# Optimization experiments

Hardware: AMD Instinct MI355X
Metric: run time of the kernel (lower is better)

Reference implementation:

```python
import jax, jax.numpy as jnp
import numpy as np

N_NODES = 50000

def _add_self_loops(edge_index, n):
    loop = jnp.arange(n, dtype=edge_index.dtype)
    src = jnp.concatenate([edge_index[0], loop])
    dst = jnp.concatenate([edge_index[1], loop])
    return src, dst

def _gcn_conv(x, src, dst, W, b, n):
    h = x @ W
    deg = jax.ops.segment_sum(jnp.ones_like(dst, dtype=h.dtype), dst, num_segments=n)
    inv_sqrt = jnp.where(deg > 0, jax.lax.rsqrt(deg), 0.0)
    coef = inv_sqrt[src] * inv_sqrt[dst]            # [E]
    msg = h[src] * coef[:, None]                     # [E, hidden]
    return jax.ops.segment_sum(msg, dst, num_segments=n) + b

def _gat_conv(x, src, dst, W, att_src, att_dst, b, n, heads, out_dim):
    # PyG GATConv, concat=False -> mean over heads; self-loops already added
    h = (x @ W).reshape(n, heads, out_dim)           # [N, H, F]
    a_src = jnp.sum(h * att_src, axis=-1)            # [N, H]
    a_dst = jnp.sum(h * att_dst, axis=-1)            # [N, H]
    e = a_src[src] + a_dst[dst]                      # [E, H]
    e = jax.nn.leaky_relu(e, negative_slope=0.2)
    # neighborhood softmax over edges grouped by destination
    m = jax.ops.segment_max(e, dst, num_segments=n)  # [N, H]
    ex = jnp.exp(e - m[dst])
    denom = jax.ops.segment_sum(ex, dst, num_segments=n)
    alpha = ex / denom[dst]                          # [E, H]
    out = jax.ops.segment_sum(h[src] * alpha[:, :, None], dst, num_segments=n)  # [N, H, F]
    return out.mean(axis=1) + b                      # concat=False -> head mean

def setup_inputs() -> dict:
    key = jax.random.key(0)
    ks = jax.random.split(key, 12)
    n, input_dim, hidden, output_dim, heads = N_NODES, 128, 128, 64, 2
    gat_out = hidden // 2
    x = jax.random.normal(ks[0], (n, input_dim), dtype=jnp.float32)
    edge_index = jax.random.randint(ks[1], (2, 800000), 0, n, dtype=jnp.int64)
    s = lambda fi, fo: float(np.sqrt(1.0 / fi))
    W1 = jax.random.normal(ks[2], (input_dim, hidden), dtype=jnp.float32) * s(input_dim, hidden)
    b1 = jnp.zeros((hidden,), dtype=jnp.float32)
    Wg = jax.random.normal(ks[3], (hidden, heads * gat_out), dtype=jnp.float32) * s(hidden, gat_out)
    att_src = jax.random.normal(ks[4], (heads, gat_out), dtype=jnp.float32) * s(gat_out, 1)
    att_dst = jax.random.normal(ks[5], (heads, gat_out), dtype=jnp.float32) * s(gat_out, 1)
    bg = jnp.zeros((gat_out,), dtype=jnp.float32)
    W3 = jax.random.normal(ks[6], (gat_out, output_dim), dtype=jnp.float32) * s(gat_out, output_dim)
    b3 = jnp.zeros((output_dim,), dtype=jnp.float32)
    return {"x": x, "edge_index": edge_index, "W1": W1, "b1": b1, "Wg": Wg,
            "att_src": att_src, "att_dst": att_dst, "bg": bg, "W3": W3, "b3": b3}

def reference(x, edge_index, W1, b1, Wg, att_src, att_dst, bg, W3, b3):
    n = x.shape[0]
    heads, gat_out = att_src.shape
    src, dst = _add_self_loops(edge_index, n)
    # dropout is identity in eval mode
    h = _gcn_conv(x, src, dst, W1, b1, n)
    h = jax.nn.relu(h)
    h = _gat_conv(h, src, dst, Wg, att_src, att_dst, bg, n, heads, gat_out)
    h = jax.nn.elu(h)
    return _gcn_conv(h, src, dst, W3, b3, n)
```

## Files before the change

### kernel.cpp

```cpp
#include <hip/hip_runtime.h>
#include <hip/hip_bf16.h>
#include <math.h>

#define N_NODES 50000
#define E0      800000
#define E_TOT   (E0 + N_NODES)
#define SCAP    512

using bf16 = __hip_bfloat16;
typedef __attribute__((ext_vector_type(8))) short bfrag;
typedef __attribute__((ext_vector_type(4))) float ffrag;

static __device__ __forceinline__ float bfu2f_lo(unsigned u){ return __uint_as_float(u << 16); }
static __device__ __forceinline__ float bfu2f_hi(unsigned u){ return __uint_as_float(u & 0xffff0000u); }
static __device__ __forceinline__ float us2f(unsigned short u){ return __uint_as_float((unsigned)u << 16); }

static __device__ __forceinline__ unsigned packbf(float a, float b){
    bf16 x = __float2bfloat16(a), y = __float2bfloat16(b);
    unsigned short ux = *reinterpret_cast<unsigned short*>(&x);
    unsigned short uy = *reinterpret_cast<unsigned short*>(&y);
    return ((unsigned)uy << 16) | ux;
}

static __device__ __forceinline__ int detect_f32(const unsigned* xu){
    int lane = threadIdx.x & 63;
    unsigned ex = (xu[lane] >> 7) & 0xFF;
    return (__ballot(ex < 100 || ex > 140) != 0ULL);
}
static __device__ __forceinline__ int detect_i32(const int* ei){
    int lane = threadIdx.x & 63;
    return (__ballot(ei[2 * lane + 1] != 0) != 0ULL);
}

static __device__ __forceinline__ float ldany(const void* p, int i, int isf32){
    return isf32 ? ((const float*)p)[i] : __bfloat162float(((const bf16*)p)[i]);
}

__global__ void k_convert(const void* __restrict__ xv,
                          const void* W1, const void* Wg, const void* W3,
                          const void* b1, const void* bg, const void* b3,
                          const void* as_, const void* ad_,
                          bf16* __restrict__ W1p, bf16* __restrict__ Wgp,
                          bf16* __restrict__ W3p, float* __restrict__ vecf,
                          bf16* __restrict__ xb, int* __restrict__ deg){
    const int NXB = (N_NODES * 128 + 255) / 256;
    int b = blockIdx.x, t = threadIdx.x;
    if (b >= 148 + NXB){
        int i = (b - 148 - NXB) * 256 + t;
        if (i < N_NODES) deg[i] = 0;
        return;
    }
    int isf = detect_f32((const unsigned*)xv);
    if (b >= 148){
        int i = (b - 148) * 256 + t;
        if (i < N_NODES * 128) xb[i] = __float2bfloat16(ldany(xv, i, isf));
        return;
    }
    if (b < 16){
        int dd = b * 256 + t;
        int j  = dd & 7;
        int L  = (dd >> 3) & 63;
        int kc = (dd >> 9) & 1;
        int ct = dd >> 10;
        int k = kc * 32 + ((L >> 4) << 3) + j;
        int n = ct * 16 + (L & 15);
        W3p[dd] = __float2bfloat16(ldany(W3, k * 64 + n, isf));
    }
    else if (b < 18){
        int i = (b - 16) * 256 + t;
        float v;
        if      (i < 128) v = ldany(b1,  i,       isf);
        else if (i < 192) v = ldany(bg,  i - 128, isf);
        else if (i < 256) v = ldany(b3,  i - 192, isf);
        else if (i < 384) v = ldany(as_, i - 256, isf);
        else              v = ldany(ad_, i - 384, isf);
        vecf[i] = v;
    } else {
        int d = (b - 18) * 256 + t;
        const void* Wsrc = (d < 16384) ? W1 : Wg;
        bf16* Wdst = (d < 16384) ? W1p : Wgp;
        int dd = d & 16383;
        int j  = dd & 7;
        int L  = (dd >> 3) & 63;
        int kc = (dd >> 9) & 3;
        int ct = dd >> 11;
        int k = kc * 32 + ((L >> 4) << 3) + j;
        int n = ct * 16 + (L & 15);
        Wdst[dd] = __float2bfloat16(ldany(Wsrc, k * 128 + n, isf));
    }
}


static __device__ __forceinline__ int load_dst(const int* ei, int e, int is32){
    if (e >= E0) return e - E0;
    return is32 ? ei[E0 + e] : (int)((const long long*)ei)[E0 + e];
}
static __device__ __forceinline__ int load_src(const int* ei, int e, int is32){
    if (e >= E0) return e - E0;
    return is32 ? ei[e] : (int)((const long long*)ei)[e];
}

__global__ void k_count(const int* __restrict__ ei, int* __restrict__ deg,
                        int* __restrict__ rank){
    int is32 = detect_i32(ei);
    int e = blockIdx.x * blockDim.x + threadIdx.x;
    if (e >= E_TOT) return;
    int dst = load_dst(ei, e, is32);
    int src = load_src(ei, e, is32);
    if ((unsigned)dst >= N_NODES || (unsigned)src >= N_NODES) return;
    rank[e] = atomicAdd(&deg[dst], 1);
}

__global__ void k_scanA(const int* __restrict__ deg, int* __restrict__ tmp, int* __restrict__ blk){
    __shared__ int s[256];
    int t = threadIdx.x;
    int i = blockIdx.x * 256 + t;
    int v = (i < N_NODES) ? deg[i] : 0;
    s[t] = v; __syncthreads();
    for (int off = 1; off < 256; off <<= 1){
        int x = (t >= off) ? s[t - off] : 0;
        __syncthreads();
        s[t] += x;
        __syncthreads();
    }
    if (t == 255) blk[blockIdx.x] = s[255];
    if (i < N_NODES) tmp[i] = s[t] - v;
}

__global__ void k_scanC(int* __restrict__ row_ptr, const int* __restrict__ blk,
                        const int* __restrict__ deg, float* __restrict__ inv_sqrt,
                        int nb){
    __shared__ int s[256];
    int t = threadIdx.x;
    int B = blockIdx.x;
    s[t] = (t < nb && t < B) ? blk[t] : 0;
    __syncthreads();
    for (int off = 128; off; off >>= 1){
        if (t < off) s[t] += s[t + off];
        __syncthreads();
    }
    int base = s[0];
    int i = B * 256 + t;
    if (i < N_NODES){
        row_ptr[i] += base;
        int d = deg[i];
        inv_sqrt[i] = (d > 0) ? rsqrtf((float)d) : 0.0f;
    }
    if (i == 0) row_ptr[N_NODES] = E_TOT;
}

__global__ void k_fill(const int* __restrict__ ei, const int* __restrict__ row_ptr,
                       const float* __restrict__ isq, const int* __restrict__ rank,
                       int2* __restrict__ ecr){
    int is32 = detect_i32(ei);
    int e = blockIdx.x * blockDim.x + threadIdx.x;
    if (e >= E_TOT) return;
    int dst = load_dst(ei, e, is32);
    int src = load_src(ei, e, is32);
    if ((unsigned)dst >= N_NODES || (unsigned)src >= N_NODES) return;
    int pos = row_ptr[dst] + rank[e];
    float c = isq[dst] * isq[src];
    ecr[pos] = make_int2(src, __float_as_int(c));
}

__global__ __launch_bounds__(256, 2) void k_gather(
        const ushort4* __restrict__ xb4, const int* __restrict__ rp,
        const int2* __restrict__ ecr, uint2* __restrict__ Xa){
    __shared__ int   scsr[SCAP];
    __shared__ float scf[SCAP];
    int n0 = blockIdx.x * 4;
    int b0 = rp[n0];
    int tot  = rp[n0 + 4] - b0;
    int stot = min(tot, SCAP);
    for (int i = threadIdx.x; i < stot; i += 256){
        int2 ev = ecr[b0 + i];
        scsr[i] = ev.x;
        scf[i]  = __int_as_float(ev.y);
    }
    __syncthreads();

    int w    = threadIdx.x >> 6;
    int half = (threadIdx.x >> 5) & 1;
    int fz   = threadIdx.x & 31;
    int n = n0 + w;
    float a0 = 0.f, a1 = 0.f, a2 = 0.f, a3 = 0.f;
    int b = rp[n] - b0, e = rp[n + 1] - b0;
    int elim = min(e, stot);
    #pragma unroll 4
    for (int i = b + half; i < elim; i += 2){
        int s = scsr[i];
        float c = scf[i];
        ushort4 v = xb4[(size_t)s * 32 + fz];
        a0 += c * us2f(v.x);  a1 += c * us2f(v.y);
        a2 += c * us2f(v.z);  a3 += c * us2f(v.w);
    }
    int start = max(b, stot);
    int i0 = start + (((b + half) ^ start) & 1);
    for (int i = i0; i < e; i += 2){
        int2 ev = ecr[b0 + i];
        float c = __int_as_float(ev.y);
        ushort4 v = xb4[(size_t)ev.x * 32 + fz];
        a0 += c * us2f(v.x);  a1 += c * us2f(v.y);
        a2 += c * us2f(v.z);  a3 += c * us2f(v.w);
    }
    a0 += __shfl_xor(a0, 32, 64);  a1 += __shfl_xor(a1, 32, 64);
    a2 += __shfl_xor(a2, 32, 64);  a3 += __shfl_xor(a3, 32, 64);
    if (half == 0)
        Xa[(size_t)n * 32 + fz] = make_uint2(packbf(a0, a1), packbf(a2, a3));
}

template<int EPI>
__global__ __launch_bounds__(512) void k_gemm_mfma(
        const bf16* __restrict__ A, const bf16* __restrict__ Wp,
        const float* __restrict__ vecf, bf16* __restrict__ O,
        float* __restrict__ aS, float* __restrict__ aD){
    __shared__ float sA[16][8];
    __shared__ float sD[16][8];
    int wid  = threadIdx.x >> 6;
    int lane = threadIdx.x & 63;
    int n0 = blockIdx.x * 16;
    int m = lane & 15, q = lane >> 4;

    const bfrag* Ap = (const bfrag*)(A + (size_t)(n0 + m) * 128);
    const bfrag* Bp = (const bfrag*)Wp + (size_t)wid * 256 + lane;

    ffrag c = {0.f, 0.f, 0.f, 0.f};
    #pragma unroll
    for (int kc = 0; kc < 4; ++kc){
        bfrag af = Ap[kc * 4 + q];
        bfrag bf = Bp[kc * 64];
        c = __builtin_amdgcn_mfma_f32_16x16x32_bf16(af, bf, c, 0, 0, 0);
    }
    __syncthreads();

    int col = wid * 16 + m;
    if (EPI == 0){
        float bb = vecf[col];
        #pragma unroll
        for (int r = 0; r < 4; ++r){
            int row = n0 + q * 4 + r;
            O[(size_t)row * 128 + col] = __float2bfloat16(fmaxf(c[r] + bb, 0.f));
        }
    } else {
        int f = col & 63, h = col >> 6;
        float as_v = vecf[256 + h * 64 + f];
        float ad_v = vecf[384 + h * 64 + f];
        float ps[4], pd[4];
        #pragma unroll
        for (int r = 0; r < 4; ++r){
            int row = n0 + q * 4 + r;
            O[(size_t)row * 128 + f * 2 + h] = __float2bfloat16(c[r]);
            ps[r] = c[r] * as_v;
            pd[r] = c[r] * ad_v;
        }
        #pragma unroll
        for (int off = 1; off < 16; off <<= 1){
            #pragma unroll
            for (int r = 0; r < 4; ++r){
                ps[r] += __shfl_xor(ps[r], off, 64);
                pd[r] += __shfl_xor(pd[r], off, 64);
            }
        }
        if (m == 0){
            #pragma unroll
            for (int r = 0; r < 4; ++r){
                int rl = q * 4 + r;
                sA[rl][wid] = ps[r];
                sD[rl][wid] = pd[r];
            }
        }
        __syncthreads();
        int t = threadIdx.x;
        if (t < 64){
            int rl = t >> 2, hh = (t >> 1) & 1, which = t & 1;
            const float (*S)[8] = which ? sD : sA;
            float v = S[rl][hh * 4 + 0] + S[rl][hh * 4 + 1]
                    + S[rl][hh * 4 + 2] + S[rl][hh * 4 + 3];
            float* dp = which ? aD : aS;
            dp[(size_t)(n0 + rl) * 2 + hh] = v;
        }
    }
}

__global__ __launch_bounds__(256) void k_gemm_z(
        const bf16* __restrict__ Y, const bf16* __restrict__ W3p,
        bf16* __restrict__ Z){
    int wid  = threadIdx.x >> 6;
    int lane = threadIdx.x & 63;
    int n0 = blockIdx.x * 16;
    int m = lane & 15, q = lane >> 4;

    const bfrag* Ap = (const bfrag*)(Y + (size_t)(n0 + m) * 64);
    const bfrag* Bp = (const bfrag*)W3p + (size_t)wid * 128 + lane;

    ffrag c = {0.f, 0.f, 0.f, 0.f};
    #pragma unroll
    for (int kc = 0; kc < 2; ++kc){
        bfrag af = Ap[kc * 4 + q];
        bfrag bf = Bp[kc * 64];
        c = __builtin_amdgcn_mfma_f32_16x16x32_bf16(af, bf, c, 0, 0, 0);
    }
    int col = wid * 16 + m;
    #pragma unroll
    for (int r = 0; r < 4; ++r){
        int row = n0 + q * 4 + r;
        Z[(size_t)row * 64 + col] = __float2bfloat16(c[r]);
    }
}

__global__ __launch_bounds__(256) void k_gat(
        const uint2* __restrict__ X2u2, const int* __restrict__ rp,
        const int2* __restrict__ ecr, const float2* __restrict__ a_src,
        const float2* __restrict__ a_dst, const float* __restrict__ vecf,
        unsigned* __restrict__ Yu){
    __shared__ int    scsr[SCAP];
    __shared__ float2 pe[SCAP];
    int n0 = blockIdx.x * 4;
    int b0 = rp[n0];
    int tot  = rp[n0 + 4] - b0;
    int stot = min(tot, SCAP);
    for (int i = threadIdx.x; i < stot; i += 256) scsr[i] = ecr[b0 + i].x;
    __syncthreads();

    int w    = threadIdx.x >> 6;
    int f    = threadIdx.x & 63;
    int half = (threadIdx.x >> 5) & 1;
    int fz   = threadIdx.x & 31;
    int n = n0 + w;
    float2 ad = a_dst[n];
    int b = rp[n] - b0, e = rp[n + 1] - b0;
    int elim = min(e, stot);

    for (int i = b + f; i < elim; i += 64){
        float2 av = a_src[scsr[i]];
        float e0 = av.x + ad.x, e1 = av.y + ad.y;
        e0 = (e0 > 0.f) ? e0 : 0.2f * e0;
        e1 = (e1 > 0.f) ? e1 : 0.2f * e1;
        pe[i] = make_float2(__expf(e0), __expf(e1));
    }

    float l0 = 0.f, l1 = 0.f;
    float o00 = 0.f, o01 = 0.f, o10 = 0.f, o11 = 0.f;
    #pragma unroll 4
    for (int i = b + half; i < elim; i += 2){
        float2 p = pe[i];
        uint2 v = X2u2[(size_t)scsr[i] * 32 + fz];
        l0  += p.x;                 l1  += p.y;
        o00 += p.x * bfu2f_lo(v.x); o01 += p.y * bfu2f_hi(v.x);
        o10 += p.x * bfu2f_lo(v.y); o11 += p.y * bfu2f_hi(v.y);
    }
    int start = max(b, stot);
    int i0 = start + (((b + half) ^ start) & 1);
    for (int i = i0; i < e; i += 2){
        int s = ecr[b0 + i].x;
        float2 av = a_src[s];
        uint2 v = X2u2[(size_t)s * 32 + fz];
        float e0 = av.x + ad.x, e1 = av.y + ad.y;
        e0 = (e0 > 0.f) ? e0 : 0.2f * e0;
        e1 = (e1 > 0.f) ? e1 : 0.2f * e1;
        float p0 = __expf(e0), p1 = __expf(e1);
        l0  += p0;                 l1  += p1;
        o00 += p0 * bfu2f_lo(v.x); o01 += p1 * bfu2f_hi(v.x);
        o10 += p0 * bfu2f_lo(v.y); o11 += p1 * bfu2f_hi(v.y);
    }
    l0  += __shfl_xor(l0, 32, 64);   l1  += __shfl_xor(l1, 32, 64);
    o00 += __shfl_xor(o00, 32, 64);  o01 += __shfl_xor(o01, 32, 64);
    o10 += __shfl_xor(o10, 32, 64);  o11 += __shfl_xor(o11, 32, 64);
    if (half == 0){
        float v0 = 0.5f * (o00 / l0 + o01 / l1) + vecf[128 + 2 * fz];
        float v1 = 0.5f * (o10 / l0 + o11 / l1) + vecf[128 + 2 * fz + 1];
        v0 = (v0 > 0.f) ? v0 : expm1f(v0);
        v1 = (v1 > 0.f) ? v1 : expm1f(v1);
        Yu[(size_t)n * 32 + fz] = packbf(v0, v1);
    }
}

__global__ __launch_bounds__(256) void k_gather_out(
        const unsigned* __restrict__ Zu, const int* __restrict__ rp,
        const int2* __restrict__ ecr, const float* __restrict__ vecf,
        float2* __restrict__ out2){
    __shared__ int   scsr[SCAP];
    __shared__ float scf[SCAP];
    int n0 = blockIdx.x * 4;
    int b0 = rp[n0];
    int tot  = rp[n0 + 4] - b0;
    int stot = min(tot, SCAP);
    for (int i = threadIdx.x; i < stot; i += 256){
        int2 ev = ecr[b0 + i];
        scsr[i] = ev.x;
        scf[i]  = __int_as_float(ev.y);
    }
    __syncthreads();

    int w    = threadIdx.x >> 6;
    int half = (threadIdx.x >> 5) & 1;
    int fz   = threadIdx.x & 31;
    int n = n0 + w;
    float a0 = 0.f, a1 = 0.f;
    int b = rp[n] - b0, e = rp[n + 1] - b0;
    int elim = min(e, stot);
    #pragma unroll 4
    for (int i = b + half; i < elim; i += 2){
        float c = scf[i];
        unsigned v = Zu[(size_t)scsr[i] * 32 + fz];
        a0 += c * bfu2f_lo(v);
        a1 += c * bfu2f_hi(v);
    }
    int start = max(b, stot);
    int i0 = start + (((b + half) ^ start) & 1);
    for (int i = i0; i < e; i += 2){
        int2 ev = ecr[b0 + i];
        float c = __int_as_float(ev.y);
        unsigned v = Zu[(size_t)ev.x * 32 + fz];
        a0 += c * bfu2f_lo(v);
        a1 += c * bfu2f_hi(v);
    }
    a0 += __shfl_xor(a0, 32, 64);
    a1 += __shfl_xor(a1, 32, 64);
    if (half == 0)
        out2[(size_t)n * 32 + fz] =
            make_float2(a0 + vecf[192 + 2 * fz], a1 + vecf[192 + 2 * fz + 1]);
}


extern "C" void kernel_launch(void* const* d_in, const int* in_sizes, int n_in,
                              void* d_out, int out_size, void* d_ws, size_t ws_size,
                              hipStream_t stream) {
    const void* x  = d_in[0];
    const int*  ei = (const int*)d_in[1];
    float* out = (float*)d_out;

    char* p = (char*)d_ws;
    auto alloc = [&](size_t bytes) -> void* {
        void* r = (void*)p;
        p += (bytes + 255) & ~(size_t)255;
        return r;
    };
    int*   deg      = (int*)  alloc((size_t)N_NODES * 4);
    int*   row_ptr  = (int*)  alloc((size_t)(N_NODES + 1) * 4);
    int*   blk      = (int*)  alloc(256 * 4);
    int*   rank     = (int*)  alloc((size_t)E_TOT * 4);
    int2*  ecr      = (int2*) alloc((size_t)E_TOT * 8);
    float* inv_sqrt = (float*)alloc((size_t)N_NODES * 4);
    float* a_src    = (float*)alloc((size_t)N_NODES * 2 * 4);
    float* a_dst    = (float*)alloc((size_t)N_NODES * 2 * 4);
    bf16*  W1p      = (bf16*) alloc(16384 * 2);
    bf16*  Wgp      = (bf16*) alloc(16384 * 2);
    bf16*  W3p      = (bf16*) alloc(4096 * 2);
    float* vecf     = (float*)alloc(512 * 4);
    bf16*  xb       = (bf16*) alloc((size_t)N_NODES * 128 * 2);
    bf16*  XA       = (bf16*) alloc((size_t)N_NODES * 128 * 2);
    bf16*  Y        = (bf16*) alloc((size_t)N_NODES * 64 * 2);
    bf16*  Z        = xb;

    const int NB_NODE = (N_NODES + 255) / 256;
    const int NB_EDGE = (E_TOT + 255) / 256;
    const int NXB     = (N_NODES * 128 + 255) / 256;
    const int NB_CONV = 148 + NXB + NB_NODE;

    k_convert<<<NB_CONV, 256, 0, stream>>>(x, d_in[2], d_in[4], d_in[8],
                                           d_in[3], d_in[7], d_in[9], d_in[5], d_in[6],
                                           W1p, Wgp, W3p, vecf, xb, deg);
    k_count<<<NB_EDGE, 256, 0, stream>>>(ei, deg, rank);
    k_scanA<<<NB_NODE, 256, 0, stream>>>(deg, row_ptr, blk);
    k_scanC<<<NB_NODE, 256, 0, stream>>>(row_ptr, blk, deg, inv_sqrt, NB_NODE);
    k_fill<<<NB_EDGE, 256, 0, stream>>>(ei, row_ptr, inv_sqrt, rank, ecr);

    k_gather<<<N_NODES / 4, 256, 0, stream>>>((const ushort4*)xb, row_ptr, ecr,
                                              (uint2*)XA);
    k_gemm_mfma<0><<<N_NODES / 16, 512, 0, stream>>>(XA, W1p, vecf, XA,
                                                     nullptr, nullptr);
    k_gemm_mfma<1><<<N_NODES / 16, 512, 0, stream>>>(XA, Wgp, vecf, XA,
                                                     a_src, a_dst);
    k_gat<<<N_NODES / 4, 256, 0, stream>>>((const uint2*)XA, row_ptr, ecr,
                                           (const float2*)a_src, (const float2*)a_dst,
                                           vecf, (unsigned*)Y);
    k_gemm_z<<<N_NODES / 16, 256, 0, stream>>>(Y, W3p, Z);
    k_gather_out<<<N_NODES / 4, 256, 0, stream>>>((const unsigned*)Z, row_ptr, ecr,
                                                  vecf, (float2*)out);
}
```

Baseline: 289.9 us.

## Widen gather loads to 16 bytes and split wave into four edge lanes

The three edge-gather kernels (GCN gather, GAT aggregation, output gather) now have each lane load wider vectors per source row (uint4 or uint2 instead of ushort4, uint2 or unsigned). The 64-lane wave is split into four groups of 16 lanes that process four edges at once, with a two-step shuffle reduction at the end. The input conversion is also vectorised to float4 loads and uint2 stores. The aim is fewer, wider memory transactions and more edge-level parallelism per wave. The cost is extra registers and shuffle work, and the gather kernel loses its explicit two-blocks-per-CU occupancy hint.

```diff
diff --git a/kernel.cpp b/kernel.cpp
--- a/kernel.cpp
+++ b/kernel.cpp
@@ -13,7 +13,6 @@
 
 static __device__ __forceinline__ float bfu2f_lo(unsigned u){ return __uint_as_float(u << 16); }
 static __device__ __forceinline__ float bfu2f_hi(unsigned u){ return __uint_as_float(u & 0xffff0000u); }
-static __device__ __forceinline__ float us2f(unsigned short u){ return __uint_as_float((unsigned)u << 16); }
 
 static __device__ __forceinline__ unsigned packbf(float a, float b){
     bf16 x = __float2bfloat16(a), y = __float2bfloat16(b);
@@ -43,7 +42,7 @@
                           bf16* __restrict__ W1p, bf16* __restrict__ Wgp,
                           bf16* __restrict__ W3p, float* __restrict__ vecf,
                           bf16* __restrict__ xb, int* __restrict__ deg){
-    const int NXB = (N_NODES * 128 + 255) / 256;
+    const int NXB = (N_NODES * 32 + 255) / 256;
     int b = blockIdx.x, t = threadIdx.x;
     if (b >= 148 + NXB){
         int i = (b - 148 - NXB) * 256 + t;
@@ -53,7 +52,14 @@
     int isf = detect_f32((const unsigned*)xv);
     if (b >= 148){
         int i = (b - 148) * 256 + t;
-        if (i < N_NODES * 128) xb[i] = __float2bfloat16(ldany(xv, i, isf));
+        if (i < N_NODES * 32){
+            if (isf){
+                float4 v = ((const float4*)xv)[i];
+                ((uint2*)xb)[i] = make_uint2(packbf(v.x, v.y), packbf(v.z, v.w));
+            } else {
+                ((uint2*)xb)[i] = ((const uint2*)xv)[i];
+            }
+        }
         return;
     }
     if (b < 16){
@@ -163,15 +169,14 @@
     ecr[pos] = make_int2(src, __float_as_int(c));
 }
 
-__global__ __launch_bounds__(256, 2) void k_gather(
-        const ushort4* __restrict__ xb4, const int* __restrict__ rp,
-        const int2* __restrict__ ecr, uint2* __restrict__ Xa){
+__global__ __launch_bounds__(256) void k_gather(
+        const uint4* __restrict__ xb16, const int* __restrict__ rp,
+        const int2* __restrict__ ecr, uint4* __restrict__ Xa16){
     __shared__ int   scsr[SCAP];
     __shared__ float scf[SCAP];
     int n0 = blockIdx.x * 4;
     int b0 = rp[n0];
-    int tot  = rp[n0 + 4] - b0;
-    int stot = min(tot, SCAP);
+    int stot = min(rp[n0 + 4] - b0, SCAP);
     for (int i = threadIdx.x; i < stot; i += 256){
         int2 ev = ecr[b0 + i];
         scsr[i] = ev.x;
@@ -179,34 +184,47 @@
     }
     __syncthreads();
 
-    int w    = threadIdx.x >> 6;
-    int half = (threadIdx.x >> 5) & 1;
-    int fz   = threadIdx.x & 31;
+    int w = threadIdx.x >> 6, lane = threadIdx.x & 63;
+    int q4 = lane >> 4, fz = lane & 15;
     int n = n0 + w;
-    float a0 = 0.f, a1 = 0.f, a2 = 0.f, a3 = 0.f;
+    float a0=0,a1=0,a2=0,a3=0,a4=0,a5=0,a6=0,a7=0;
     int b = rp[n] - b0, e = rp[n + 1] - b0;
     int elim = min(e, stot);
-    #pragma unroll 4
-    for (int i = b + half; i < elim; i += 2){
+    #pragma unroll 2
+    for (int i = b + q4; i < elim; i += 4){
         int s = scsr[i];
         float c = scf[i];
-        ushort4 v = xb4[(size_t)s * 32 + fz];
-        a0 += c * us2f(v.x);  a1 += c * us2f(v.y);
-        a2 += c * us2f(v.z);  a3 += c * us2f(v.w);
+        uint4 v = xb16[(size_t)s * 16 + fz];
+        a0 += c * bfu2f_lo(v.x);  a1 += c * bfu2f_hi(v.x);
+        a2 += c * bfu2f_lo(v.y);  a3 += c * bfu2f_hi(v.y);
+        a4 += c * bfu2f_lo(v.z);  a5 += c * bfu2f_hi(v.z);
+        a6 += c * bfu2f_lo(v.w);  a7 += c * bfu2f_hi(v.w);
     }
     int start = max(b, stot);
-    int i0 = start + (((b + half) ^ start) & 1);
-    for (int i = i0; i < e; i += 2){
+    int i0 = start + (((b + q4) - start) & 3);
+    for (int i = i0; i < e; i += 4){
         int2 ev = ecr[b0 + i];
         float c = __int_as_float(ev.y);
-        ushort4 v = xb4[(size_t)ev.x * 32 + fz];
-        a0 += c * us2f(v.x);  a1 += c * us2f(v.y);
-        a2 += c * us2f(v.z);  a3 += c * us2f(v.w);
-    }
-    a0 += __shfl_xor(a0, 32, 64);  a1 += __shfl_xor(a1, 32, 64);
-    a2 += __shfl_xor(a2, 32, 64);  a3 += __shfl_xor(a3, 32, 64);
-    if (half == 0)
-        Xa[(size_t)n * 32 + fz] = make_uint2(packbf(a0, a1), packbf(a2, a3));
+        uint4 v = xb16[(size_t)ev.x * 16 + fz];
+        a0 += c * bfu2f_lo(v.x);  a1 += c * bfu2f_hi(v.x);
+        a2 += c * bfu2f_lo(v.y);  a3 += c * bfu2f_hi(v.y);
+        a4 += c * bfu2f_lo(v.z);  a5 += c * bfu2f_hi(v.z);
+        a6 += c * bfu2f_lo(v.w);  a7 += c * bfu2f_hi(v.w);
+    }
+    a0 += __shfl_xor(a0, 32, 64);  a0 += __shfl_xor(a0, 16, 64);
+    a1 += __shfl_xor(a1, 32, 64);  a1 += __shfl_xor(a1, 16, 64);
+    a2 += __shfl_xor(a2, 32, 64);  a2 += __shfl_xor(a2, 16, 64);
+    a3 += __shfl_xor(a3, 32, 64);  a3 += __shfl_xor(a3, 16, 64);
+    a4 += __shfl_xor(a4, 32, 64);  a4 += __shfl_xor(a4, 16, 64);
+    a5 += __shfl_xor(a5, 32, 64);  a5 += __shfl_xor(a5, 16, 64);
+    a6 += __shfl_xor(a6, 32, 64);  a6 += __shfl_xor(a6, 16, 64);
+    a7 += __shfl_xor(a7, 32, 64);  a7 += __shfl_xor(a7, 16, 64);
+    if (lane < 16){
+        uint4 o;
+        o.x = packbf(a0, a1);  o.y = packbf(a2, a3);
+        o.z = packbf(a4, a5);  o.w = packbf(a6, a7);
+        Xa16[(size_t)n * 16 + fz] = o;
+    }
 }
 
 template<int EPI>
@@ -309,29 +327,26 @@
 }
 
 __global__ __launch_bounds__(256) void k_gat(
-        const uint2* __restrict__ X2u2, const int* __restrict__ rp,
+        const uint4* __restrict__ X2v, const int* __restrict__ rp,
         const int2* __restrict__ ecr, const float2* __restrict__ a_src,
         const float2* __restrict__ a_dst, const float* __restrict__ vecf,
-        unsigned* __restrict__ Yu){
+        uint2* __restrict__ Yu2){
     __shared__ int    scsr[SCAP];
     __shared__ float2 pe[SCAP];
     int n0 = blockIdx.x * 4;
     int b0 = rp[n0];
-    int tot  = rp[n0 + 4] - b0;
-    int stot = min(tot, SCAP);
+    int stot = min(rp[n0 + 4] - b0, SCAP);
     for (int i = threadIdx.x; i < stot; i += 256) scsr[i] = ecr[b0 + i].x;
     __syncthreads();
 
-    int w    = threadIdx.x >> 6;
-    int f    = threadIdx.x & 63;
-    int half = (threadIdx.x >> 5) & 1;
-    int fz   = threadIdx.x & 31;
+    int w = threadIdx.x >> 6, lane = threadIdx.x & 63;
+    int q4 = lane >> 4, fz = lane & 15;
     int n = n0 + w;
     float2 ad = a_dst[n];
     int b = rp[n] - b0, e = rp[n + 1] - b0;
     int elim = min(e, stot);
 
-    for (int i = b + f; i < elim; i += 64){
+    for (int i = b + lane; i < elim; i += 64){
         float2 av = a_src[scsr[i]];
         float e0 = av.x + ad.x, e1 = av.y + ad.y;
         e0 = (e0 > 0.f) ? e0 : 0.2f * e0;
@@ -340,21 +355,23 @@
     }
 
     float l0 = 0.f, l1 = 0.f;
-    float o00 = 0.f, o01 = 0.f, o10 = 0.f, o11 = 0.f;
-    #pragma unroll 4
-    for (int i = b + half; i < elim; i += 2){
+    float o00=0,o01=0, o10=0,o11=0, o20=0,o21=0, o30=0,o31=0;
+    #pragma unroll 2
+    for (int i = b + q4; i < elim; i += 4){
         float2 p = pe[i];
-        uint2 v = X2u2[(size_t)scsr[i] * 32 + fz];
-        l0  += p.x;                 l1  += p.y;
-        o00 += p.x * bfu2f_lo(v.x); o01 += p.y * bfu2f_hi(v.x);
-        o10 += p.x * bfu2f_lo(v.y); o11 += p.y * bfu2f_hi(v.y);
+        uint4 v = X2v[(size_t)scsr[i] * 16 + fz];
+        l0  += p.x;                  l1  += p.y;
+        o00 += p.x * bfu2f_lo(v.x);  o01 += p.y * bfu2f_hi(v.x);
+        o10 += p.x * bfu2f_lo(v.y);  o11 += p.y * bfu2f_hi(v.y);
+        o20 += p.x * bfu2f_lo(v.z);  o21 += p.y * bfu2f_hi(v.z);
+        o30 += p.x * bfu2f_lo(v.w);  o31 += p.y * bfu2f_hi(v.w);
     }
     int start = max(b, stot);
-    int i0 = start + (((b + half) ^ start) & 1);
-    for (int i = i0; i < e; i += 2){
+    int i0 = start + (((b + q4) - start) & 3);
+    for (int i = i0; i < e; i += 4){
         int s = ecr[b0 + i].x;
         float2 av = a_src[s];
-        uint2 v = X2u2[(size_t)s * 32 + fz];
+        uint4 v = X2v[(size_t)s * 16 + fz];
         float e0 = av.x + ad.x, e1 = av.y + ad.y;
         e0 = (e0 > 0.f) ? e0 : 0.2f * e0;
         e1 = (e1 > 0.f) ? e1 : 0.2f * e1;
@@ -362,29 +379,41 @@
         l0  += p0;                 l1  += p1;
         o00 += p0 * bfu2f_lo(v.x); o01 += p1 * bfu2f_hi(v.x);
         o10 += p0 * bfu2f_lo(v.y); o11 += p1 * bfu2f_hi(v.y);
-    }
-    l0  += __shfl_xor(l0, 32, 64);   l1  += __shfl_xor(l1, 32, 64);
-    o00 += __shfl_xor(o00, 32, 64);  o01 += __shfl_xor(o01, 32, 64);
-    o10 += __shfl_xor(o10, 32, 64);  o11 += __shfl_xor(o11, 32, 64);
-    if (half == 0){
-        float v0 = 0.5f * (o00 / l0 + o01 / l1) + vecf[128 + 2 * fz];
-        float v1 = 0.5f * (o10 / l0 + o11 / l1) + vecf[128 + 2 * fz + 1];
+        o20 += p0 * bfu2f_lo(v.z); o21 += p1 * bfu2f_hi(v.z);
+        o30 += p0 * bfu2f_lo(v.w); o31 += p1 * bfu2f_hi(v.w);
+    }
+    l0  += __shfl_xor(l0, 32, 64);   l0  += __shfl_xor(l0, 16, 64);
+    l1  += __shfl_xor(l1, 32, 64);   l1  += __shfl_xor(l1, 16, 64);
+    o00 += __shfl_xor(o00, 32, 64);  o00 += __shfl_xor(o00, 16, 64);
+    o01 += __shfl_xor(o01, 32, 64);  o01 += __shfl_xor(o01, 16, 64);
+    o10 += __shfl_xor(o10, 32, 64);  o10 += __shfl_xor(o10, 16, 64);
+    o11 += __shfl_xor(o11, 32, 64);  o11 += __shfl_xor(o11, 16, 64);
+    o20 += __shfl_xor(o20, 32, 64);  o20 += __shfl_xor(o20, 16, 64);
+    o21 += __shfl_xor(o21, 32, 64);  o21 += __shfl_xor(o21, 16, 64);
+    o30 += __shfl_xor(o30, 32, 64);  o30 += __shfl_xor(o30, 16, 64);
+    o31 += __shfl_xor(o31, 32, 64);  o31 += __shfl_xor(o31, 16, 64);
+    if (lane < 16){
+        float v0 = 0.5f * (o00 / l0 + o01 / l1) + vecf[128 + 4 * fz + 0];
+        float v1 = 0.5f * (o10 / l0 + o11 / l1) + vecf[128 + 4 * fz + 1];
+        float v2 = 0.5f * (o20 / l0 + o21 / l1) + vecf[128 + 4 * fz + 2];
+        float v3 = 0.5f * (o30 / l0 + o31 / l1) + vecf[128 + 4 * fz + 3];
         v0 = (v0 > 0.f) ? v0 : expm1f(v0);
         v1 = (v1 > 0.f) ? v1 : expm1f(v1);
-        Yu[(size_t)n * 32 + fz] = packbf(v0, v1);
+        v2 = (v2 > 0.f) ? v2 : expm1f(v2);
+        v3 = (v3 > 0.f) ? v3 : expm1f(v3);
+        Yu2[(size_t)n * 16 + fz] = make_uint2(packbf(v0, v1), packbf(v2, v3));
     }
 }
 
 __global__ __launch_bounds__(256) void k_gather_out(
-        const unsigned* __restrict__ Zu, const int* __restrict__ rp,
+        const uint2* __restrict__ Zu2, const int* __restrict__ rp,
         const int2* __restrict__ ecr, const float* __restrict__ vecf,
-        float2* __restrict__ out2){
+        float4* __restrict__ out4){
     __shared__ int   scsr[SCAP];
     __shared__ float scf[SCAP];
     int n0 = blockIdx.x * 4;
     int b0 = rp[n0];
-    int tot  = rp[n0 + 4] - b0;
-    int stot = min(tot, SCAP);
+    int stot = min(rp[n0 + 4] - b0, SCAP);
     for (int i = threadIdx.x; i < stot; i += 256){
         int2 ev = ecr[b0 + i];
         scsr[i] = ev.x;
@@ -392,34 +421,36 @@
     }
     __syncthreads();
 
-    int w    = threadIdx.x >> 6;
-    int half = (threadIdx.x >> 5) & 1;
-    int fz   = threadIdx.x & 31;
+    int w = threadIdx.x >> 6, lane = threadIdx.x & 63;
+    int q4 = lane >> 4, fz = lane & 15;
     int n = n0 + w;
-    float a0 = 0.f, a1 = 0.f;
+    float a0 = 0.f, a1 = 0.f, a2 = 0.f, a3 = 0.f;
     int b = rp[n] - b0, e = rp[n + 1] - b0;
     int elim = min(e, stot);
-    #pragma unroll 4
-    for (int i = b + half; i < elim; i += 2){
+    #pragma unroll 2
+    for (int i = b + q4; i < elim; i += 4){
         float c = scf[i];
-        unsigned v = Zu[(size_t)scsr[i] * 32 + fz];
-        a0 += c * bfu2f_lo(v);
-        a1 += c * bfu2f_hi(v);
+        uint2 v = Zu2[(size_t)scsr[i] * 16 + fz];
+        a0 += c * bfu2f_lo(v.x);  a1 += c * bfu2f_hi(v.x);
+        a2 += c * bfu2f_lo(v.y);  a3 += c * bfu2f_hi(v.y);
     }
     int start = max(b, stot);
-    int i0 = start + (((b + half) ^ start) & 1);
-    for (int i = i0; i < e; i += 2){
+    int i0 = start + (((b + q4) - start) & 3);
+    for (int i = i0; i < e; i += 4){
         int2 ev = ecr[b0 + i];
         float c = __int_as_float(ev.y);
-        unsigned v = Zu[(size_t)ev.x * 32 + fz];
-        a0 += c * bfu2f_lo(v);
-        a1 += c * bfu2f_hi(v);
-    }
-    a0 += __shfl_xor(a0, 32, 64);
-    a1 += __shfl_xor(a1, 32, 64);
-    if (half == 0)
-        out2[(size_t)n * 32 + fz] =
-            make_float2(a0 + vecf[192 + 2 * fz], a1 + vecf[192 + 2 * fz + 1]);
+        uint2 v = Zu2[(size_t)ev.x * 16 + fz];
+        a0 += c * bfu2f_lo(v.x);  a1 += c * bfu2f_hi(v.x);
+        a2 += c * bfu2f_lo(v.y);  a3 += c * bfu2f_hi(v.y);
+    }
+    a0 += __shfl_xor(a0, 32, 64);  a0 += __shfl_xor(a0, 16, 64);
+    a1 += __shfl_xor(a1, 32, 64);  a1 += __shfl_xor(a1, 16, 64);
+    a2 += __shfl_xor(a2, 32, 64);  a2 += __shfl_xor(a2, 16, 64);
+    a3 += __shfl_xor(a3, 32, 64);  a3 += __shfl_xor(a3, 16, 64);
+    if (lane < 16)
+        out4[(size_t)n * 16 + fz] = make_float4(
+            a0 + vecf[192 + 4 * fz + 0], a1 + vecf[192 + 4 * fz + 1],
+            a2 + vecf[192 + 4 * fz + 2], a3 + vecf[192 + 4 * fz + 3]);
 }
 
 
@@ -455,7 +486,7 @@
 
     const int NB_NODE = (N_NODES + 255) / 256;
     const int NB_EDGE = (E_TOT + 255) / 256;
-    const int NXB     = (N_NODES * 128 + 255) / 256;
+    const int NXB     = (N_NODES * 32 + 255) / 256;
     const int NB_CONV = 148 + NXB + NB_NODE;
 
     k_convert<<<NB_CONV, 256, 0, stream>>>(x, d_in[2], d_in[4], d_in[8],
@@ -466,16 +497,16 @@
     k_scanC<<<NB_NODE, 256, 0, stream>>>(row_ptr, blk, deg, inv_sqrt, NB_NODE);
     k_fill<<<NB_EDGE, 256, 0, stream>>>(ei, row_ptr, inv_sqrt, rank, ecr);
 
-    k_gather<<<N_NODES / 4, 256, 0, stream>>>((const ushort4*)xb, row_ptr, ecr,
-                                              (uint2*)XA);
+    k_gather<<<N_NODES / 4, 256, 0, stream>>>((const uint4*)xb, row_ptr, ecr,
+                                              (uint4*)XA);
     k_gemm_mfma<0><<<N_NODES / 16, 512, 0, stream>>>(XA, W1p, vecf, XA,
                                                      nullptr, nullptr);
     k_gemm_mfma<1><<<N_NODES / 16, 512, 0, stream>>>(XA, Wgp, vecf, XA,
                                                      a_src, a_dst);
-    k_gat<<<N_NODES / 4, 256, 0, stream>>>((const uint2*)XA, row_ptr, ecr,
+    k_gat<<<N_NODES / 4, 256, 0, stream>>>((const uint4*)XA, row_ptr, ecr,
                                            (const float2*)a_src, (const float2*)a_dst,
-                                           vecf, (unsigned*)Y);
+                                           vecf, (uint2*)Y);
     k_gemm_z<<<N_NODES / 16, 256, 0, stream>>>(Y, W3p, Z);
-    k_gather_out<<<N_NODES / 4, 256, 0, stream>>>((const unsigned*)Z, row_ptr, ecr,
-                                                  vecf, (float2*)out);
-}
+    k_gather_out<<<N_NODES / 4, 256, 0, stream>>>((const uint2*)Z, row_ptr, ecr,
+                                                  vecf, (float4*)out);
+}
```

After: 285.4 us. No clear change (-1.5%).
